# Kernel tuning notes

Hardware: AMD Instinct MI355X
Metric: run time of the kernel (lower is better)

Reference implementation:

```python
import jax, jax.numpy as jnp
import numpy as np

DIM = 768
EPS = 1e-06


def _layernorm(x, gamma, beta):
    # LayerNorm over last axis (channels), eps=EPS, elementwise affine
    mu = jnp.mean(x, axis=-1, keepdims=True)
    var = jnp.mean(jnp.square(x - mu), axis=-1, keepdims=True)
    return (x - mu) * jax.lax.rsqrt(var + EPS) * gamma + beta


def setup_inputs() -> dict:
    key = jax.random.key(0)
    ks = jax.random.split(key, 10)
    B, C, H, W = 16, DIM, 32, 32
    s = 1.0 / np.sqrt(C)  # mimic Conv2d default init scale
    return {
        "x": jax.random.normal(ks[0], (B, C, H, W), dtype=jnp.float32),
        "W1": jax.random.uniform(ks[1], (C, C), jnp.float32, -s, s),
        "b1": jax.random.uniform(ks[2], (C,), jnp.float32, -s, s),
        "g1": jnp.ones((C,), jnp.float32),
        "beta1": jnp.zeros((C,), jnp.float32),
        "W2": jax.random.uniform(ks[3], (C, C), jnp.float32, -s, s),
        "b2": jax.random.uniform(ks[4], (C,), jnp.float32, -s, s),
        "g2": jnp.ones((C,), jnp.float32),
        "beta2": jnp.zeros((C,), jnp.float32),
        "W3": jax.random.uniform(ks[5], (C, C), jnp.float32, -s, s),
        "b3": jax.random.uniform(ks[6], (C,), jnp.float32, -s, s),
    }


def reference(x, W1, b1, g1, beta1, W2, b2, g2, beta2, W3, b3):
    # x: [B, C, H, W] (NCHW). Work in NHWC; 1x1 conv == channel matmul.
    h = jnp.transpose(x, (0, 2, 3, 1))  # [B, H, W, C]
    h = jnp.einsum("bhwc,oc->bhwo", h, W1) + b1
    h = jax.nn.gelu(_layernorm(h, g1, beta1), approximate=False)
    h = jnp.einsum("bhwc,oc->bhwo", h, W2) + b2
    h = jax.nn.gelu(_layernorm(h, g2, beta2), approximate=False)
    h = jnp.einsum("bhwc,oc->bhwo", h, W3) + b3
    return jnp.transpose(h, (0, 3, 1, 2))  # back to NCHW
```

## Files before the change

kernel.cpp:

```cpp
#include <hip/hip_runtime.h>
#include <hip/hip_bf16.h>

typedef __bf16 bf16;
typedef __bf16 bf16x4 __attribute__((ext_vector_type(4)));
typedef __bf16 bf16x8 __attribute__((ext_vector_type(8)));
typedef float f32x4 __attribute__((ext_vector_type(4)));

#define DIM 768
#define HW 1024
#define BATCH 16
#define M_TOTAL (BATCH * HW)
#define NKT 12

#define AS1 __attribute__((address_space(1)))
#define AS3 __attribute__((address_space(3)))


__global__ void prep_kernel(const float* __restrict__ x, bf16* __restrict__ xb,
                            const float4* __restrict__ w1, const float4* __restrict__ w2,
                            const float4* __restrict__ w3,
                            bf16x8* __restrict__ o1, bf16x8* __restrict__ o2,
                            bf16x8* __restrict__ o3) {
    __shared__ float tile[32][33];
    if (blockIdx.x < 864) {
        const int b = blockIdx.x;
        const int which = b / 288;
        const int i = (b % 288) * 256 + threadIdx.x;
        const float4* w = which == 0 ? w1 : which == 1 ? w2 : w3;
        bf16x8* o = which == 0 ? o1 : which == 1 ? o2 : o3;
        const int row = i / 96, br = i % 96;
        const int q = br >> 2, g = br & 3;
        float4 lo = w[row * 192 + q * 8 + g];
        float4 hi = w[row * 192 + q * 8 + g + 4];
        bf16x8 r = { (bf16)lo.x, (bf16)lo.y, (bf16)lo.z, (bf16)lo.w,
                     (bf16)hi.x, (bf16)hi.y, (bf16)hi.z, (bf16)hi.w };
        o[row * 96 + br] = r;
    } else {
        const int e = blockIdx.x - 864;
        const int b = e / 768;
        const int rem = e % 768;
        const int c0 = (rem / 32) * 32;
        const int hw0 = (rem % 32) * 32;
        const int tx = threadIdx.x & 31, ty = threadIdx.x >> 5;

        const float* src = x + ((size_t)b * DIM + c0) * HW + hw0;
#pragma unroll
        for (int j = 0; j < 4; j++)
            tile[ty + 8 * j][tx] = src[(size_t)(ty + 8 * j) * HW + tx];
        __syncthreads();
        const int ptx = (((tx & 15) >> 2) << 3) + (tx & 3) + ((tx >> 4) << 2);
        bf16* dst = xb + ((size_t)b * HW + hw0) * DIM + c0;
#pragma unroll
        for (int j = 0; j < 4; j++)
            dst[(size_t)(ty + 8 * j) * DIM + ptx] = (bf16)tile[tx][ty + 8 * j];
    }
}

template <int MODE>
__global__ __launch_bounds__(512, 2) void gemm_kernel(
    const bf16* __restrict__ A,
    const bf16* __restrict__ Bw,
    const float* __restrict__ bias,
    void* __restrict__ out)
{
    constexpr int K = DIM;
    __shared__ bf16 lds[2][2][256][64];

    const int t = threadIdx.x;
    const int lane = t & 63;
    const int wave = t >> 6;
    const int wm = wave >> 2, wn = wave & 3;

    const int bid = blockIdx.x;
    const int swz = (bid & 7) * 24 + (bid >> 3);
    const int m0 = (swz % 64) * 256;
    const int n0 = (swz / 64) * 256;

    const int fr = lane & 15;
    const int fq = lane >> 4;

    f32x4 acc[8][4] = {};

    const int s_r = t >> 3;
    const int s_blk = t & 7;

    auto stage_half = [&](int kt, int which, int half) {
        const int d = kt & 1;
        const bf16* src = which == 0 ? A : Bw;
        const int row0 = which == 0 ? m0 : n0;
#pragma unroll
        for (int j = 0; j < 2; j++) {
            const int r = s_r + j * 64;
            const int R = half * 128 + r;
            __builtin_amdgcn_global_load_lds(
                (const AS1 void*)(src + (size_t)(row0 + R) * K + kt * 64 + ((s_blk ^ (r & 7)) << 3)),
                (AS3 void*)&lds[d][which][R][s_blk * 8], 16, 0, 0);
        }
    };

    bf16x8 a[8], b0[4], b1[4];

    auto ldA = [&](int kt, int mh) {
        const int d = kt & 1;
#pragma unroll
        for (int mi = 0; mi < 4; mi++) {
            const int R = wm * 128 + (mh * 4 + mi) * 16 + fr;
            const bf16* rp = &lds[d][0][R][0];
            const int s = R & 7;
#pragma unroll
            for (int ks = 0; ks < 2; ks++)
                a[mi * 2 + ks] = *(const bf16x8*)(rp + (((ks * 4 + fq) ^ s) << 3));
        }
    };
    auto ldB = [&](bf16x8* bb, int kt, int nh) {
        const int d = kt & 1;
#pragma unroll
        for (int ni = 0; ni < 2; ni++) {
            const int R = wn * 64 + (nh * 2 + ni) * 16 + fr;
            const bf16* rp = &lds[d][1][R][0];
            const int s = R & 7;
#pragma unroll
            for (int ks = 0; ks < 2; ks++)
                bb[ni * 2 + ks] = *(const bf16x8*)(rp + (((ks * 4 + fq) ^ s) << 3));
        }
    };
    auto MM = [&](bf16x8* bb, int mh, int nh) {
        __builtin_amdgcn_s_setprio(1);
#pragma unroll
        for (int mi = 0; mi < 4; mi++)
#pragma unroll
            for (int ni = 0; ni < 2; ni++)
#pragma unroll
                for (int ks = 0; ks < 2; ks++)
                    acc[mh * 4 + mi][nh * 2 + ni] = __builtin_amdgcn_mfma_f32_16x16x32_bf16(
                        a[mi * 2 + ks], bb[ni * 2 + ks], acc[mh * 4 + mi][nh * 2 + ni], 0, 0, 0);
        __builtin_amdgcn_s_setprio(0);
    };

    stage_half(0, 0, 0); stage_half(0, 0, 1); stage_half(0, 1, 0); stage_half(0, 1, 1);
    stage_half(1, 0, 0);
    asm volatile("s_waitcnt vmcnt(2)" ::: "memory");
    __builtin_amdgcn_s_barrier();

    for (int kt = 0; kt < NKT; ++kt) {
        ldA(kt, 0);
        ldB(b0, kt, 0);
        if (kt + 1 < NKT) stage_half(kt + 1, 0, 1);
        asm volatile("s_waitcnt lgkmcnt(0)" ::: "memory");
        MM(b0, 0, 0);

        ldB(b1, kt, 1);
        if (kt + 1 < NKT) stage_half(kt + 1, 1, 0);
        asm volatile("s_waitcnt lgkmcnt(0)" ::: "memory");
        MM(b1, 0, 1);

        ldA(kt, 1);
        if (kt + 1 < NKT) stage_half(kt + 1, 1, 1);
        asm volatile("s_waitcnt lgkmcnt(0)" ::: "memory");
        MM(b1, 1, 1);

        __builtin_amdgcn_s_barrier();
        if (kt + 2 < NKT) stage_half(kt + 2, 0, 0);
        MM(b0, 1, 0);

        if (kt < NKT - 2) {
            asm volatile("s_waitcnt vmcnt(2)" ::: "memory");
            __builtin_amdgcn_s_barrier();
        } else if (kt == NKT - 2) {
            asm volatile("s_waitcnt vmcnt(0)" ::: "memory");
            __builtin_amdgcn_s_barrier();
        }
        __builtin_amdgcn_sched_barrier(0);
    }

    const int fq4 = fq * 4;
    if (MODE == 0) {
        bf16* o = (bf16*)out;
#pragma unroll
        for (int mi = 0; mi < 8; mi++) {
            const int row = m0 + wm * 128 + mi * 16 + fq4;
#pragma unroll
            for (int ni = 0; ni < 4; ni++) {
                const int col = n0 + wn * 64 + ni * 16 + fr;
                const int pcol = n0 + wn * 64 + ((ni >> 1) << 5)
                               + ((fr >> 2) << 3) + (fr & 3) + ((ni & 1) << 2);
                const float bv = bias[col];
#pragma unroll
                for (int r = 0; r < 4; r++)
                    o[(size_t)(row + r) * DIM + pcol] = (bf16)(acc[mi][ni][r] + bv);
            }
        }
    } else {
        float* o = (float*)out;
#pragma unroll
        for (int mi = 0; mi < 8; mi++) {
            const int nb = m0 + wm * 128 + mi * 16 + fq4;
            const int bI = nb >> 10, hw = nb & 1023;
#pragma unroll
            for (int ni = 0; ni < 4; ni++) {
                const int col = n0 + wn * 64 + ni * 16 + fr;
                f32x4 v = acc[mi][ni] + bias[col];
                *(f32x4*)(o + ((size_t)bI * DIM + col) * HW + hw) = v;
            }
        }
    }
}

__global__ __launch_bounds__(256) void ln_gelu_kernel(
    bf16* __restrict__ h, const float* __restrict__ g, const float* __restrict__ beta)
{
    const int wave = threadIdx.x >> 6;
    const int lane = threadIdx.x & 63;
    const int n = blockIdx.x * 4 + wave;
    bf16* row = h + (size_t)n * DIM;

    float v[12];
    float s = 0.f, ss = 0.f;
#pragma unroll
    for (int j = 0; j < 3; j++) {
        bf16x4 x = *(const bf16x4*)(row + j * 256 + lane * 4);
#pragma unroll
        for (int i = 0; i < 4; i++) {
            float f = (float)x[i];
            v[j * 4 + i] = f;
            s += f;
            ss += f * f;
        }
    }
#pragma unroll
    for (int off = 32; off > 0; off >>= 1) {
        s += __shfl_xor(s, off);
        ss += __shfl_xor(ss, off);
    }
    const float mu = s * (1.f / DIM);
    const float var = ss * (1.f / DIM) - mu * mu;
    const float rstd = rsqrtf(var + 1e-6f);

#pragma unroll
    for (int j = 0; j < 3; j++) {
        bf16x4 r;
#pragma unroll
        for (int i = 0; i < 4; i++) {
            const int c = j * 256 + lane * 4 + i;
            const int p = (lane * 4 + i) & 31;
            const int kk = ((p >> 3) << 2) + (p & 7) + ((p & 4) ? 12 : 0);
            const int gi = (c & ~31) + kk;
            float y = (v[j * 4 + i] - mu) * rstd * g[gi] + beta[gi];
            y = 0.5f * y * (1.f + erff(y * 0.70710678118f));
            r[i] = (bf16)y;
        }
        *(bf16x4*)(row + j * 256 + lane * 4) = r;
    }
}

extern "C" void kernel_launch(void* const* d_in, const int* in_sizes, int n_in,
                              void* d_out, int out_size, void* d_ws, size_t ws_size,
                              hipStream_t stream) {
    const float* x   = (const float*)d_in[0];
    const float* W1  = (const float*)d_in[1];
    const float* b1  = (const float*)d_in[2];
    const float* g1  = (const float*)d_in[3];
    const float* be1 = (const float*)d_in[4];
    const float* W2  = (const float*)d_in[5];
    const float* b2  = (const float*)d_in[6];
    const float* g2  = (const float*)d_in[7];
    const float* be2 = (const float*)d_in[8];
    const float* W3  = (const float*)d_in[9];
    const float* b3  = (const float*)d_in[10];
    float* out = (float*)d_out;

    bf16* Wb1  = (bf16*)d_ws;
    bf16* Wb2  = Wb1 + (size_t)DIM * DIM;
    bf16* Wb3  = Wb2 + (size_t)DIM * DIM;
    bf16* buf0 = Wb3 + (size_t)DIM * DIM;
    bf16* buf1 = buf0 + (size_t)M_TOTAL * DIM;

    prep_kernel<<<864 + 12288, 256, 0, stream>>>(
        x, buf0, (const float4*)W1, (const float4*)W2, (const float4*)W3,
        (bf16x8*)Wb1, (bf16x8*)Wb2, (bf16x8*)Wb3);

    const int ggrid = (M_TOTAL / 256) * (DIM / 256);
    gemm_kernel<0><<<ggrid, 512, 0, stream>>>(buf0, Wb1, b1, buf1);
    ln_gelu_kernel<<<M_TOTAL / 4, 256, 0, stream>>>(buf1, g1, be1);
    gemm_kernel<0><<<ggrid, 512, 0, stream>>>(buf1, Wb2, b2, buf0);
    ln_gelu_kernel<<<M_TOTAL / 4, 256, 0, stream>>>(buf0, g2, be2);
    gemm_kernel<1><<<ggrid, 512, 0, stream>>>(buf0, Wb3, b3, out);
}
```

Measured before the change: 150.7 us.

## Retile GEMM to 256x192 blocks so the grid fills every CU

Shrinks the GEMM block tile along N from 256 to 192, which raises the grid from 192 to 256 workgroups so every CU on the device gets one. The B tile in LDS, the accumulator array and the output column permutation are resized to match. The staging of global-to-LDS loads is rewritten into seven 64-row chunks spread across the K-loop phases, and the MFMA phases are regrouped around a single B fragment load. The trade-off is less data reuse per block, since each A tile is now reloaded four times instead of three.

```diff
diff --git a/kernel.cpp b/kernel.cpp
--- a/kernel.cpp
+++ b/kernel.cpp
@@ -64,7 +64,8 @@
     void* __restrict__ out)
 {
     constexpr int K = DIM;
-    __shared__ bf16 lds[2][2][256][64];
+    __shared__ bf16 ldsA[2][256][64];
+    __shared__ bf16 ldsB[2][192][64];
 
     const int t = threadIdx.x;
     const int lane = t & 63;
@@ -72,96 +73,94 @@
     const int wm = wave >> 2, wn = wave & 3;
 
     const int bid = blockIdx.x;
-    const int swz = (bid & 7) * 24 + (bid >> 3);
-    const int m0 = (swz % 64) * 256;
-    const int n0 = (swz / 64) * 256;
+    const int virt = (bid & 7) * 32 + (bid >> 3);
+    const int m0 = (virt >> 2) * 256;
+    const int n0 = (virt & 3) * 192;
 
     const int fr = lane & 15;
     const int fq = lane >> 4;
 
-    f32x4 acc[8][4] = {};
+    f32x4 acc[8][3] = {};
 
     const int s_r = t >> 3;
     const int s_blk = t & 7;
 
-    auto stage_half = [&](int kt, int which, int half) {
+    auto stage_chunk = [&](int kt, int c) {
         const int d = kt & 1;
-        const bf16* src = which == 0 ? A : Bw;
-        const int row0 = which == 0 ? m0 : n0;
-#pragma unroll
-        for (int j = 0; j < 2; j++) {
-            const int r = s_r + j * 64;
-            const int R = half * 128 + r;
+        if (c < 4) {
+            const int r = c * 64 + s_r;
             __builtin_amdgcn_global_load_lds(
-                (const AS1 void*)(src + (size_t)(row0 + R) * K + kt * 64 + ((s_blk ^ (r & 7)) << 3)),
-                (AS3 void*)&lds[d][which][R][s_blk * 8], 16, 0, 0);
-        }
-    };
-
-    bf16x8 a[8], b0[4], b1[4];
+                (const AS1 void*)(A + (size_t)(m0 + r) * K + kt * 64 + ((s_blk ^ (r & 7)) << 3)),
+                (AS3 void*)&ldsA[d][r][s_blk * 8], 16, 0, 0);
+        } else {
+            const int r = (c - 4) * 64 + s_r;
+            __builtin_amdgcn_global_load_lds(
+                (const AS1 void*)(Bw + (size_t)(n0 + r) * K + kt * 64 + ((s_blk ^ (r & 7)) << 3)),
+                (AS3 void*)&ldsB[d][r][s_blk * 8], 16, 0, 0);
+        }
+    };
+
+    bf16x8 a[8], b[6];
 
     auto ldA = [&](int kt, int mh) {
         const int d = kt & 1;
 #pragma unroll
         for (int mi = 0; mi < 4; mi++) {
             const int R = wm * 128 + (mh * 4 + mi) * 16 + fr;
-            const bf16* rp = &lds[d][0][R][0];
+            const bf16* rp = &ldsA[d][R][0];
             const int s = R & 7;
 #pragma unroll
             for (int ks = 0; ks < 2; ks++)
                 a[mi * 2 + ks] = *(const bf16x8*)(rp + (((ks * 4 + fq) ^ s) << 3));
         }
     };
-    auto ldB = [&](bf16x8* bb, int kt, int nh) {
+    auto ldB = [&](int kt) {
         const int d = kt & 1;
 #pragma unroll
-        for (int ni = 0; ni < 2; ni++) {
-            const int R = wn * 64 + (nh * 2 + ni) * 16 + fr;
-            const bf16* rp = &lds[d][1][R][0];
+        for (int j = 0; j < 3; j++) {
+            const int R = wn * 48 + j * 16 + fr;
+            const bf16* rp = &ldsB[d][R][0];
             const int s = R & 7;
 #pragma unroll
             for (int ks = 0; ks < 2; ks++)
-                bb[ni * 2 + ks] = *(const bf16x8*)(rp + (((ks * 4 + fq) ^ s) << 3));
-        }
-    };
-    auto MM = [&](bf16x8* bb, int mh, int nh) {
+                b[j * 2 + ks] = *(const bf16x8*)(rp + (((ks * 4 + fq) ^ s) << 3));
+        }
+    };
+    auto MM = [&](int mh, int j0, int j1) {
         __builtin_amdgcn_s_setprio(1);
 #pragma unroll
         for (int mi = 0; mi < 4; mi++)
 #pragma unroll
-            for (int ni = 0; ni < 2; ni++)
-#pragma unroll
-                for (int ks = 0; ks < 2; ks++)
-                    acc[mh * 4 + mi][nh * 2 + ni] = __builtin_amdgcn_mfma_f32_16x16x32_bf16(
-                        a[mi * 2 + ks], bb[ni * 2 + ks], acc[mh * 4 + mi][nh * 2 + ni], 0, 0, 0);
+            for (int j = 0; j < 3; j++)
+                if (j >= j0 && j < j1)
+#pragma unroll
+                    for (int ks = 0; ks < 2; ks++)
+                        acc[mh * 4 + mi][j] = __builtin_amdgcn_mfma_f32_16x16x32_bf16(
+                            a[mi * 2 + ks], b[j * 2 + ks], acc[mh * 4 + mi][j], 0, 0, 0);
         __builtin_amdgcn_s_setprio(0);
     };
 
-    stage_half(0, 0, 0); stage_half(0, 0, 1); stage_half(0, 1, 0); stage_half(0, 1, 1);
-    stage_half(1, 0, 0);
+#pragma unroll
+    for (int c = 0; c < 7; c++) stage_chunk(0, c);
+    stage_chunk(1, 0); stage_chunk(1, 1);
     asm volatile("s_waitcnt vmcnt(2)" ::: "memory");
     __builtin_amdgcn_s_barrier();
 
     for (int kt = 0; kt < NKT; ++kt) {
         ldA(kt, 0);
-        ldB(b0, kt, 0);
-        if (kt + 1 < NKT) stage_half(kt + 1, 0, 1);
+        ldB(kt);
+        if (kt + 1 < NKT) { stage_chunk(kt + 1, 2); stage_chunk(kt + 1, 3); stage_chunk(kt + 1, 4); }
         asm volatile("s_waitcnt lgkmcnt(0)" ::: "memory");
-        MM(b0, 0, 0);
-
-        ldB(b1, kt, 1);
-        if (kt + 1 < NKT) stage_half(kt + 1, 1, 0);
+        MM(0, 0, 3);
+
+        ldA(kt, 1);
+        if (kt + 1 < NKT) { stage_chunk(kt + 1, 5); stage_chunk(kt + 1, 6); }
         asm volatile("s_waitcnt lgkmcnt(0)" ::: "memory");
-        MM(b1, 0, 1);
-
-        ldA(kt, 1);
-        if (kt + 1 < NKT) stage_half(kt + 1, 1, 1);
-        asm volatile("s_waitcnt lgkmcnt(0)" ::: "memory");
-        MM(b1, 1, 1);
+        MM(1, 0, 2);
 
         __builtin_amdgcn_s_barrier();
-        if (kt + 2 < NKT) stage_half(kt + 2, 0, 0);
-        MM(b0, 1, 0);
+        if (kt + 2 < NKT) { stage_chunk(kt + 2, 0); stage_chunk(kt + 2, 1); }
+        MM(1, 2, 3);
 
         if (kt < NKT - 2) {
             asm volatile("s_waitcnt vmcnt(2)" ::: "memory");
@@ -180,14 +179,15 @@
         for (int mi = 0; mi < 8; mi++) {
             const int row = m0 + wm * 128 + mi * 16 + fq4;
 #pragma unroll
-            for (int ni = 0; ni < 4; ni++) {
-                const int col = n0 + wn * 64 + ni * 16 + fr;
-                const int pcol = n0 + wn * 64 + ((ni >> 1) << 5)
-                               + ((fr >> 2) << 3) + (fr & 3) + ((ni & 1) << 2);
-                const float bv = bias[col];
+            for (int j = 0; j < 3; j++) {
+                const int gcol = n0 + wn * 48 + j * 16 + fr;
+                const int kk = gcol & 31;
+                const int pcol = (gcol & ~31) + (((kk & 15) >> 2) << 3) + (kk & 3)
+                               + ((kk >> 4) << 2);
+                const float bv = bias[gcol];
 #pragma unroll
                 for (int r = 0; r < 4; r++)
-                    o[(size_t)(row + r) * DIM + pcol] = (bf16)(acc[mi][ni][r] + bv);
+                    o[(size_t)(row + r) * DIM + pcol] = (bf16)(acc[mi][j][r] + bv);
             }
         }
     } else {
@@ -197,9 +197,9 @@
             const int nb = m0 + wm * 128 + mi * 16 + fq4;
             const int bI = nb >> 10, hw = nb & 1023;
 #pragma unroll
-            for (int ni = 0; ni < 4; ni++) {
-                const int col = n0 + wn * 64 + ni * 16 + fr;
-                f32x4 v = acc[mi][ni] + bias[col];
+            for (int j = 0; j < 3; j++) {
+                const int col = n0 + wn * 48 + j * 16 + fr;
+                f32x4 v = acc[mi][j] + bias[col];
                 *(f32x4*)(o + ((size_t)bI * DIM + col) * HW + hw) = v;
             }
         }
@@ -279,7 +279,7 @@
         x, buf0, (const float4*)W1, (const float4*)W2, (const float4*)W3,
         (bf16x8*)Wb1, (bf16x8*)Wb2, (bf16x8*)Wb3);
 
-    const int ggrid = (M_TOTAL / 256) * (DIM / 256);
+    const int ggrid = (M_TOTAL / 256) * (DIM / 192);
     gemm_kernel<0><<<ggrid, 512, 0, stream>>>(buf0, Wb1, b1, buf1);
     ln_gelu_kernel<<<M_TOTAL / 4, 256, 0, stream>>>(buf1, g1, be1);
     gemm_kernel<0><<<ggrid, 512, 0, stream>>>(buf1, Wb2, b2, buf0);
```

Measured after the change: 142.1 us. 1.06x faster.
